# Performance work log

Measured on AMD Instinct MI355X. Metric: run time of the kernel, lower is better.

Reference implementation:

```python
import jax, jax.numpy as jnp
import numpy as np

N = 50000
E = 800000
IN_CH = 128
HIDDEN = 32
HEADS = 4
OUT_CH = 64
NEG_SLOPE = 0.2


def setup_inputs() -> dict:
    key = jax.random.key(0)
    ks = jax.random.split(key, 12)
    x = jax.random.normal(ks[0], (N, IN_CH), dtype=jnp.float32)
    edge_index = jax.random.randint(ks[1], (2, E), 0, N, dtype=jnp.int64)
    # layer 1: GATConv(IN_CH, HIDDEN, heads=4, concat=True)
    s1 = 1.0 / np.sqrt(IN_CH)
    W1 = jax.random.normal(ks[2], (IN_CH, HEADS * HIDDEN), dtype=jnp.float32) * s1
    att_src1 = jax.random.normal(ks[3], (HEADS, HIDDEN), dtype=jnp.float32) * 0.1
    att_dst1 = jax.random.normal(ks[4], (HEADS, HIDDEN), dtype=jnp.float32) * 0.1
    b1 = jnp.zeros((HEADS * HIDDEN,), dtype=jnp.float32)
    # layer 2: GATConv(HEADS*HIDDEN, OUT_CH, heads=1, concat=False)
    s2 = 1.0 / np.sqrt(HEADS * HIDDEN)
    W2 = jax.random.normal(ks[5], (HEADS * HIDDEN, OUT_CH), dtype=jnp.float32) * s2
    att_src2 = jax.random.normal(ks[6], (1, OUT_CH), dtype=jnp.float32) * 0.1
    att_dst2 = jax.random.normal(ks[7], (1, OUT_CH), dtype=jnp.float32) * 0.1
    b2 = jnp.zeros((OUT_CH,), dtype=jnp.float32)
    return {"x": x, "edge_index": edge_index, "W1": W1, "att_src1": att_src1,
            "att_dst1": att_dst1, "b1": b1, "W2": W2, "att_src2": att_src2,
            "att_dst2": att_dst2, "b2": b2}


def gat_conv(x, src, dst, W, a_src, a_dst, bias, heads, out_ch, concat):
    n = x.shape[0]
    h = (x @ W).reshape(n, heads, out_ch)               # [N, H, C]
    alpha_s = jnp.sum(h * a_src[None], axis=-1)          # [N, H]
    alpha_d = jnp.sum(h * a_dst[None], axis=-1)          # [N, H]
    e = alpha_s[src] + alpha_d[dst]                      # [E, H]
    e = jnp.where(e > 0, e, NEG_SLOPE * e)               # leaky_relu(0.2)
    # segment softmax over incoming edges of each dst node
    e_max = jax.ops.segment_max(e, dst, num_segments=n)
    e_max = jnp.where(jnp.isfinite(e_max), e_max, 0.0)
    ex = jnp.exp(e - e_max[dst])
    denom = jax.ops.segment_sum(ex, dst, num_segments=n)
    alpha = ex / (denom[dst] + 1e-16)                    # [E, H]
    msg = h[src] * alpha[:, :, None]                     # [E, H, C]
    out = jax.ops.segment_sum(msg, dst, num_segments=n)  # [N, H, C]
    if concat:
        out = out.reshape(n, heads * out_ch)
    else:
        out = out.mean(axis=1)
    return out + bias


def reference(x, edge_index, W1, att_src1, att_dst1, b1, W2, att_src2, att_dst2, b2):
    n = x.shape[0]
    loop = jnp.arange(n, dtype=edge_index.dtype)
    src = jnp.concatenate([edge_index[0], loop])  # add self-loops (PyG default)
    dst = jnp.concatenate([edge_index[1], loop])
    h = gat_conv(x, src, dst, W1, att_src1, att_dst1, b1, HEADS, HIDDEN, True)
    h = jax.nn.elu(h)
    return gat_conv(h, src, dst, W2, att_src2, att_dst2, b2, 1, OUT_CH, False)
```

## Files before the change

### kernel.cpp

```cpp
#include <hip/hip_runtime.h>

#define NN    50000
#define NE    800000
#define NET   850000
#define NBUCK ((NN + 255) / 256)
#define MAXB  8192

typedef __fp16 half2_t __attribute__((ext_vector_type(2)));
typedef _Float16 half8 __attribute__((ext_vector_type(8)));
typedef float floatx4 __attribute__((ext_vector_type(4)));

__device__ __forceinline__ float lrelu(float v) { return fmaxf(v, 0.2f * v); }
__device__ __forceinline__ unsigned pk16(float a, float b) {
    half2_t h = __builtin_amdgcn_cvt_pkrtz(a, b);
    return __builtin_bit_cast(unsigned, h);
}
__device__ __forceinline__ float2 unpk16(unsigned u) {
    half2_t h = __builtin_bit_cast(half2_t, u);
    return make_float2((float)h.x, (float)h.y);
}

__global__ __launch_bounds__(256) void gemm1_mfma_kernel(
    const float* __restrict__ x, const _Float16* __restrict__ w1t,
    const float* __restrict__ att_s, const float* __restrict__ att_d,
    _Float16* __restrict__ h1h, float* __restrict__ as, float* __restrict__ ad)
{
    __shared__ _Float16 hs[64 * 128];
    const int t    = threadIdx.x;
    const int lane = t & 63;
    const int m    = lane & 15;
    const int q    = lane >> 4;
    const int wv   = t >> 6;
    const int gr0  = blockIdx.x * 64;
    const int rbase = gr0 + wv * 16;

    const int rme = rbase + m;
    const int rc  = rme < NN ? rme : NN - 1;
    const float* ap = x + (size_t)rc * 128 + q * 8;

    floatx4 acc[8];
#pragma unroll
    for (int nt = 0; nt < 8; nt++) acc[nt] = (floatx4){0.f, 0.f, 0.f, 0.f};

#pragma unroll
    for (int ks = 0; ks < 4; ks++) {
        const float4 f0 = *(const float4*)(ap + ks * 32);
        const float4 f1 = *(const float4*)(ap + ks * 32 + 4);
        const uint4 au = make_uint4(pk16(f0.x, f0.y), pk16(f0.z, f0.w),
                                    pk16(f1.x, f1.y), pk16(f1.z, f1.w));
        const half8 a = __builtin_bit_cast(half8, au);
#pragma unroll
        for (int nt = 0; nt < 8; nt++) {
            const half8 b = *(const half8*)(w1t + (nt * 16 + m) * 128 + ks * 32 + q * 8);
            acc[nt] = __builtin_amdgcn_mfma_f32_16x16x32_f16(a, b, acc[nt], 0, 0, 0);
        }
    }

    const int lrow0 = wv * 16 + q * 4;
#pragma unroll
    for (int nt = 0; nt < 8; nt++)
#pragma unroll
        for (int r = 0; r < 4; r++)
            hs[(lrow0 + r) * 128 + nt * 16 + m] = (_Float16)acc[nt][r];
    __syncthreads();

#pragma unroll
    for (int i = t; i < 1024; i += 256) {
        const int row = i >> 4;
        if (gr0 + row < NN)
            ((half8*)h1h)[(size_t)(gr0 + row) * 16 + (i & 15)] = ((const half8*)hs)[i];
    }

    const int arow = t >> 2, hd = t & 3;
    const int grow = gr0 + arow;
    float ps = 0.f, pd = 0.f;
    const half8*  hp8 = (const half8*)(hs + arow * 128 + hd * 32);
    const float4* s4  = (const float4*)(att_s + hd * 32);
    const float4* d4  = (const float4*)(att_d + hd * 32);
#pragma unroll
    for (int cc = 0; cc < 4; cc++) {
        const half8 hv = hp8[cc];
        const float4 a = s4[cc * 2], b = s4[cc * 2 + 1];
        const float4 c = d4[cc * 2], e = d4[cc * 2 + 1];
        ps += (float)hv[0]*a.x + (float)hv[1]*a.y + (float)hv[2]*a.z + (float)hv[3]*a.w
            + (float)hv[4]*b.x + (float)hv[5]*b.y + (float)hv[6]*b.z + (float)hv[7]*b.w;
        pd += (float)hv[0]*c.x + (float)hv[1]*c.y + (float)hv[2]*c.z + (float)hv[3]*c.w
            + (float)hv[4]*e.x + (float)hv[5]*e.y + (float)hv[6]*e.z + (float)hv[7]*e.w;
    }
    if (grow < NN) {
        as[grow * 4 + hd] = ps;
        ad[grow * 4 + hd] = pd;
    }
}

__global__ __launch_bounds__(256) void gemm2_mfma_kernel(
    const _Float16* __restrict__ ah, const _Float16* __restrict__ w2t,
    const float* __restrict__ att_s, const float* __restrict__ att_d,
    _Float16* __restrict__ h2h, float* __restrict__ as, float* __restrict__ ad)
{
    __shared__ _Float16 hs[64 * 64];
    const int t    = threadIdx.x;
    const int lane = t & 63;
    const int m    = lane & 15;
    const int q    = lane >> 4;
    const int wv   = t >> 6;
    const int gr0  = blockIdx.x * 64;
    const int rbase = gr0 + wv * 16;

    const int rme = rbase + m;
    const int rc  = rme < NN ? rme : NN - 1;
    const _Float16* ap = ah + (size_t)rc * 128 + q * 8;

    floatx4 acc[4];
#pragma unroll
    for (int nt = 0; nt < 4; nt++) acc[nt] = (floatx4){0.f, 0.f, 0.f, 0.f};

#pragma unroll
    for (int ks = 0; ks < 4; ks++) {
        const half8 a = *(const half8*)(ap + ks * 32);
#pragma unroll
        for (int nt = 0; nt < 4; nt++) {
            const half8 b = *(const half8*)(w2t + (nt * 16 + m) * 128 + ks * 32 + q * 8);
            acc[nt] = __builtin_amdgcn_mfma_f32_16x16x32_f16(a, b, acc[nt], 0, 0, 0);
        }
    }

    const int lrow0 = wv * 16 + q * 4;
#pragma unroll
    for (int nt = 0; nt < 4; nt++)
#pragma unroll
        for (int r = 0; r < 4; r++)
            hs[(lrow0 + r) * 64 + nt * 16 + m] = (_Float16)acc[nt][r];
    __syncthreads();

#pragma unroll
    for (int i = t; i < 512; i += 256) {
        const int row = i >> 3;
        if (gr0 + row < NN)
            ((half8*)h2h)[(size_t)(gr0 + row) * 8 + (i & 7)] = ((const half8*)hs)[i];
    }

    const int arow = t >> 2, sg = t & 3;
    const int grow = gr0 + arow;
    float ps = 0.f, pd = 0.f;
    const half8*  hp8 = (const half8*)(hs + arow * 64 + sg * 16);
    const float4* s4  = (const float4*)(att_s + sg * 16);
    const float4* d4  = (const float4*)(att_d + sg * 16);
#pragma unroll
    for (int cc = 0; cc < 2; cc++) {
        const half8 hv = hp8[cc];
        const float4 a = s4[cc * 2], b = s4[cc * 2 + 1];
        const float4 c = d4[cc * 2], e = d4[cc * 2 + 1];
        ps += (float)hv[0]*a.x + (float)hv[1]*a.y + (float)hv[2]*a.z + (float)hv[3]*a.w
            + (float)hv[4]*b.x + (float)hv[5]*b.y + (float)hv[6]*b.z + (float)hv[7]*b.w;
        pd += (float)hv[0]*c.x + (float)hv[1]*c.y + (float)hv[2]*c.z + (float)hv[3]*c.w
            + (float)hv[4]*e.x + (float)hv[5]*e.y + (float)hv[6]*e.z + (float)hv[7]*e.w;
    }
    ps += __shfl_down(ps, 2);  pd += __shfl_down(pd, 2);
    ps += __shfl_down(ps, 1);  pd += __shfl_down(pd, 1);
    if (sg == 0 && grow < NN) { as[grow] = ps; ad[grow] = pd; }
}

__global__ __launch_bounds__(1024) void bin_kernel(const int* __restrict__ ei,
                                                   const float* __restrict__ W1,
                                                   const float* __restrict__ W2,
                                                   _Float16* __restrict__ w1t,
                                                   _Float16* __restrict__ w2t,
                                                   int* __restrict__ bcnt,
                                                   unsigned* __restrict__ pairs)
{
    if (blockIdx.x < 24) {
        const int idx = blockIdx.x * 1024 + threadIdx.x;
        if (idx < 16384) {
            const int k = idx >> 7, n = idx & 127;
            w1t[n * 128 + k] = (_Float16)W1[idx];
        } else {
            const int j = idx - 16384;
            const int k = j >> 6, n = j & 63;
            w2t[n * 128 + k] = (_Float16)W2[j];
        }
    }

    __shared__ int hist[NBUCK], base[NBUCK], cur[NBUCK];
    const int t = threadIdx.x;
    if (t < NBUCK) { hist[t] = 0; cur[t] = 0; }
    __syncthreads();
    const int e = blockIdx.x * 1024 + t;
    int s = 0, d = 0, bk = 0;
    const bool ok = e < NET;
    if (ok) {
        if (e < NE) { s = ei[e]; d = ei[NE + e]; } else { s = d = e - NE; }
        bk = d >> 8;
        atomicAdd(&hist[bk], 1);
    }
    __syncthreads();
    if (t < NBUCK && hist[t]) base[t] = atomicAdd(&bcnt[t], hist[t]);
    __syncthreads();
    if (ok) {
        const int r = atomicAdd(&cur[bk], 1);
        pairs[(size_t)bk * MAXB + base[bk] + r] =
            (unsigned)s | ((unsigned)(d & 255) << 16);
    }
}

__global__ __launch_bounds__(1024) void bsort_kernel(
    const int* __restrict__ bcnt, const unsigned* __restrict__ pairs,
    int* __restrict__ row_beg, int* __restrict__ row_end,
    int* __restrict__ col)
{
    __shared__ int hist[256], cur[256], sh[256];
    __shared__ int outl[MAXB];
    const int b = blockIdx.x, t = threadIdx.x;
    const int m = bcnt[b];
    const int gbase = b * MAXB;
    if (t < 256) hist[t] = 0;
    __syncthreads();
    for (int i = t; i < m; i += 1024)
        atomicAdd(&hist[pairs[gbase + i] >> 16], 1);
    __syncthreads();
    if (t < 256) sh[t] = hist[t];
    __syncthreads();
#pragma unroll
    for (int off = 1; off < 256; off <<= 1) {
        int u = (t < 256 && t >= off) ? sh[t - off] : 0;
        __syncthreads();
        if (t < 256) sh[t] += u;
        __syncthreads();
    }
    if (t < 256) {
        const int ex = sh[t] - hist[t];
        cur[t] = ex;
        const int node = (b << 8) + t;
        if (node < NN) {
            row_beg[node] = gbase + ex;
            row_end[node] = gbase + ex + hist[t];
        }
    }
    __syncthreads();
    for (int i = t; i < m; i += 1024) {
        const unsigned p = pairs[gbase + i];
        const int r = atomicAdd(&cur[p >> 16], 1);
        outl[r] = (int)(p & 0xFFFFu);
    }
    __syncthreads();
    for (int i = t; i < m; i += 1024) col[gbase + i] = outl[i];
}

__global__ __launch_bounds__(256) void agg1_fused_kernel(
    const int* __restrict__ row_beg, const int* __restrict__ row_end,
    const int* __restrict__ col, const unsigned* __restrict__ hh,
    const float* __restrict__ as1, const float* __restrict__ ad1,
    const float* __restrict__ b1, unsigned* __restrict__ acth)
{
    __shared__ float wbuf[4][64 * 4];
    const int wv   = threadIdx.x >> 6;
    const int d    = __builtin_amdgcn_readfirstlane((blockIdx.x * 256 + threadIdx.x) >> 6);
    const int lane = threadIdx.x & 63;
    const int head = lane >> 4;
    const int beg = row_beg[d], end = row_end[d];
    const float4 ad4 = ((const float4*)ad1)[d];
    float* wb = wbuf[wv];

    float acc0 = 0.f, acc1 = 0.f, den = 0.f;

    for (int jb = beg; jb < end; jb += 64) {
        const int cnt = min(64, end - jb);
        {
            const int sl = col[jb + min(lane, cnt - 1)];
            const float4 a = ((const float4*)as1)[sl];
            float4 w4;
            w4.x = __expf(lrelu(a.x + ad4.x));
            w4.y = __expf(lrelu(a.y + ad4.y));
            w4.z = __expf(lrelu(a.z + ad4.z));
            w4.w = __expf(lrelu(a.w + ad4.w));
            ((float4*)wb)[lane] = w4;
        }
        __asm__ volatile("s_waitcnt lgkmcnt(0)" ::: "memory");

        int k = 0;
        for (; k + 16 <= cnt; k += 16) {
            float    w[16];
            unsigned g[16];
#pragma unroll
            for (int u = 0; u < 16; u++) {
                const int s = col[jb + k + u];
                w[u] = wb[(k + u) * 4 + head];
                g[u] = hh[s * 64 + lane];
            }
#pragma unroll
            for (int u = 0; u < 16; u++) {
                const float2 g2 = unpk16(g[u]);
                den  += w[u];
                acc0 += w[u] * g2.x;
                acc1 += w[u] * g2.y;
            }
        }
        for (; k + 4 <= cnt; k += 4) {
            float    w[4];
            unsigned g[4];
#pragma unroll
            for (int u = 0; u < 4; u++) {
                const int s = col[jb + k + u];
                w[u] = wb[(k + u) * 4 + head];
                g[u] = hh[s * 64 + lane];
            }
#pragma unroll
            for (int u = 0; u < 4; u++) {
                const float2 g2 = unpk16(g[u]);
                den  += w[u];
                acc0 += w[u] * g2.x;
                acc1 += w[u] * g2.y;
            }
        }
        for (; k < cnt; k++) {
            const float w = wb[k * 4 + head];
            const float2 g2 = unpk16(hh[col[jb + k] * 64 + lane]);
            den  += w;
            acc0 += w * g2.x;
            acc1 += w * g2.y;
        }
        __asm__ volatile("" ::: "memory");
    }
    const float2 bb  = ((const float2*)b1)[lane];
    const float  inv = 1.f / (den + 1e-16f);
    float v0 = acc0 * inv + bb.x;
    float v1 = acc1 * inv + bb.y;
    v0 = v0 > 0.f ? v0 : (__expf(v0) - 1.f);
    v1 = v1 > 0.f ? v1 : (__expf(v1) - 1.f);
    acth[d * 64 + lane] = pk16(v0, v1);
}

__global__ __launch_bounds__(256) void agg2_fused_kernel(
    const int* __restrict__ row_beg, const int* __restrict__ row_end,
    const int* __restrict__ col, const _Float16* __restrict__ h,
    const float* __restrict__ as2, const float* __restrict__ ad2,
    const float* __restrict__ b2, float* __restrict__ out)
{
    __shared__ float wbuf[4][64];
    const int wv   = threadIdx.x >> 6;
    const int d    = __builtin_amdgcn_readfirstlane((blockIdx.x * 256 + threadIdx.x) >> 6);
    const int lane = threadIdx.x & 63;
    const int beg = row_beg[d], end = row_end[d];
    const float add = ad2[d];
    float* wb = wbuf[wv];

    float acc = 0.f, den = 0.f;

    for (int jb = beg; jb < end; jb += 64) {
        const int cnt = min(64, end - jb);
        {
            const int sl = col[jb + min(lane, cnt - 1)];
            wb[lane] = __expf(lrelu(as2[sl] + add));
        }
        __asm__ volatile("s_waitcnt lgkmcnt(0)" ::: "memory");

        int k = 0;
        for (; k + 16 <= cnt; k += 16) {
            float w[16], g[16];
#pragma unroll
            for (int u = 0; u < 16; u++) {
                const int s = col[jb + k + u];
                w[u] = wb[k + u];
                g[u] = (float)h[s * 64 + lane];
            }
#pragma unroll
            for (int u = 0; u < 16; u++) {
                den += w[u];
                acc += w[u] * g[u];
            }
        }
        for (; k + 4 <= cnt; k += 4) {
            float w[4], g[4];
#pragma unroll
            for (int u = 0; u < 4; u++) {
                const int s = col[jb + k + u];
                w[u] = wb[k + u];
                g[u] = (float)h[s * 64 + lane];
            }
#pragma unroll
            for (int u = 0; u < 4; u++) {
                den += w[u];
                acc += w[u] * g[u];
            }
        }
        for (; k < cnt; k++) {
            const float w = wb[k];
            den += w;
            acc += w * (float)h[col[jb + k] * 64 + lane];
        }
        __asm__ volatile("" ::: "memory");
    }
    out[d * 64 + lane] = acc / (den + 1e-16f) + b2[lane];
}

extern "C" void kernel_launch(void* const* d_in, const int* in_sizes, int n_in,
                              void* d_out, int out_size, void* d_ws, size_t ws_size,
                              hipStream_t stream)
{
    const float* x    = (const float*)d_in[0];
    const int*   ei   = (const int*)  d_in[1];
    const float* W1   = (const float*)d_in[2];
    const float* at_s1= (const float*)d_in[3];
    const float* at_d1= (const float*)d_in[4];
    const float* b1   = (const float*)d_in[5];
    const float* W2   = (const float*)d_in[6];
    const float* at_s2= (const float*)d_in[7];
    const float* at_d2= (const float*)d_in[8];
    const float* b2   = (const float*)d_in[9];
    float*       out  = (float*)d_out;

    const size_t NPAD = (size_t)NBUCK * MAXB;

    float* fw   = (float*)d_ws;
    float* as1  = fw;
    float* ad1  = as1  + NN * 4;
    float* as2  = ad1  + NN * 4;
    float* ad2  = as2  + NN;
    _Float16* h1h   = (_Float16*)(ad2 + NN);
    _Float16* act1h = h1h  + (size_t)NN * 128;
    _Float16* h2h   = act1h+ (size_t)NN * 128;
    _Float16* w1t   = h2h  + (size_t)NN * 64;
    _Float16* w2t   = w1t  + 16384;
    int*   row_beg = (int*)(w2t + 8192);
    int*   row_end = row_beg + NN;
    int*   col     = row_end + NN;
    int*   bcnt    = col + NPAD;
    unsigned* pairs = (unsigned*)(bcnt + 256);

    hipMemsetAsync(bcnt, 0, 256 * sizeof(int), stream);

    const int eg1024 = (NET + 1023) / 1024;
    const int gemm_grid = (NN + 63) / 64;
    const int node_wave_grid = NN / 4;

    bin_kernel  <<<eg1024, 1024, 0, stream>>>(ei, W1, W2, w1t, w2t, bcnt, pairs);
    bsort_kernel<<<NBUCK, 1024, 0, stream>>>(bcnt, pairs, row_beg, row_end, col);

    gemm1_mfma_kernel<<<gemm_grid, 256, 0, stream>>>(x, w1t, at_s1, at_d1, h1h, as1, ad1);
    agg1_fused_kernel<<<node_wave_grid, 256, 0, stream>>>(row_beg, row_end, col,
                        (const unsigned*)h1h, as1, ad1, b1, (unsigned*)act1h);

    gemm2_mfma_kernel<<<gemm_grid, 256, 0, stream>>>(act1h, w2t, at_s2, at_d2, h2h, as2, ad2);
    agg2_fused_kernel<<<node_wave_grid, 256, 0, stream>>>(row_beg, row_end, col,
                        h2h, as2, ad2, b2, out);
}
```

Before: 211.5 us.

## Split each wavefront across four edges with wide vector gathers in aggregation

Both aggregation kernels now split each 64-lane wavefront into four 16-lane groups. Each group processes a different incoming edge and gathers that source row with one 16-byte load (layer 1) or one 8-byte load (layer 2) per lane, instead of every lane loading a single 4-byte or 2-byte element for every edge. Per-lane accumulators are then combined across the groups with xor shuffles before normalisation, bias and ELU. The aim is fewer, wider gather instructions and more edges in flight per wavefront. In exchange it needs more accumulator registers, adds a cross-lane reduction, and pads the tail edges with zero weight.

Measured after the change: 213.0 us. Within noise of the previous version (+0.7%).

```diff
diff --git a/kernel.cpp b/kernel.cpp
--- a/kernel.cpp
+++ b/kernel.cpp
@@ -256,12 +256,16 @@
     const int wv   = threadIdx.x >> 6;
     const int d    = __builtin_amdgcn_readfirstlane((blockIdx.x * 256 + threadIdx.x) >> 6);
     const int lane = threadIdx.x & 63;
-    const int head = lane >> 4;
+    const int c    = lane & 15;
+    const int p    = lane >> 4;
+    const int head = c >> 2;
     const int beg = row_beg[d], end = row_end[d];
     const float4 ad4 = ((const float4*)ad1)[d];
     float* wb = wbuf[wv];
 
-    float acc0 = 0.f, acc1 = 0.f, den = 0.f;
+    float acc0 = 0.f, acc1 = 0.f, acc2 = 0.f, acc3 = 0.f;
+    float acc4 = 0.f, acc5 = 0.f, acc6 = 0.f, acc7 = 0.f;
+    float den = 0.f;
 
     for (int jb = beg; jb < end; jb += 64) {
         const int cnt = min(64, end - jb);
@@ -279,55 +283,82 @@
 
         int k = 0;
         for (; k + 16 <= cnt; k += 16) {
-            float    w[16];
-            unsigned g[16];
-#pragma unroll
-            for (int u = 0; u < 16; u++) {
-                const int s = col[jb + k + u];
-                w[u] = wb[(k + u) * 4 + head];
-                g[u] = hh[s * 64 + lane];
+            float w[4];
+            uint4 g[4];
+#pragma unroll
+            for (int u = 0; u < 4; u++) {
+                const int e0 = jb + k + 4 * u;
+                const int sA = col[e0], sB = col[e0 + 1];
+                const int sC = col[e0 + 2], sD = col[e0 + 3];
+                int s  = (p & 1) ? sB : sA;
+                const int s2 = (p & 1) ? sD : sC;
+                s = (p & 2) ? s2 : s;
+                w[u] = wb[(k + 4 * u + p) * 4 + head];
+                g[u] = *(const uint4*)(hh + (size_t)s * 64 + 4 * c);
             }
 #pragma unroll
-            for (int u = 0; u < 16; u++) {
-                const float2 g2 = unpk16(g[u]);
+            for (int u = 0; u < 4; u++) {
+                const float2 g0 = unpk16(g[u].x), g1 = unpk16(g[u].y);
+                const float2 g2 = unpk16(g[u].z), g3 = unpk16(g[u].w);
                 den  += w[u];
-                acc0 += w[u] * g2.x;
-                acc1 += w[u] * g2.y;
+                acc0 += w[u] * g0.x;  acc1 += w[u] * g0.y;
+                acc2 += w[u] * g1.x;  acc3 += w[u] * g1.y;
+                acc4 += w[u] * g2.x;  acc5 += w[u] * g2.y;
+                acc6 += w[u] * g3.x;  acc7 += w[u] * g3.y;
             }
         }
-        for (; k + 4 <= cnt; k += 4) {
-            float    w[4];
-            unsigned g[4];
-#pragma unroll
-            for (int u = 0; u < 4; u++) {
-                const int s = col[jb + k + u];
-                w[u] = wb[(k + u) * 4 + head];
-                g[u] = hh[s * 64 + lane];
-            }
-#pragma unroll
-            for (int u = 0; u < 4; u++) {
-                const float2 g2 = unpk16(g[u]);
-                den  += w[u];
-                acc0 += w[u] * g2.x;
-                acc1 += w[u] * g2.y;
-            }
-        }
-        for (; k < cnt; k++) {
-            const float w = wb[k * 4 + head];
-            const float2 g2 = unpk16(hh[col[jb + k] * 64 + lane]);
+        for (; k < cnt; k += 4) {
+            const int sA = col[jb + k];
+            const int sB = col[jb + min(k + 1, cnt - 1)];
+            const int sC = col[jb + min(k + 2, cnt - 1)];
+            const int sD = col[jb + min(k + 3, cnt - 1)];
+            int s  = (p & 1) ? sB : sA;
+            const int s2 = (p & 1) ? sD : sC;
+            s = (p & 2) ? s2 : s;
+            const float w = (k + p < cnt) ? wb[(k + p) * 4 + head] : 0.f;
+            const uint4 gv = *(const uint4*)(hh + (size_t)s * 64 + 4 * c);
+            const float2 g0 = unpk16(gv.x), g1 = unpk16(gv.y);
+            const float2 g2 = unpk16(gv.z), g3 = unpk16(gv.w);
             den  += w;
-            acc0 += w * g2.x;
-            acc1 += w * g2.y;
+            acc0 += w * g0.x;  acc1 += w * g0.y;
+            acc2 += w * g1.x;  acc3 += w * g1.y;
+            acc4 += w * g2.x;  acc5 += w * g2.y;
+            acc6 += w * g3.x;  acc7 += w * g3.y;
         }
         __asm__ volatile("" ::: "memory");
     }
-    const float2 bb  = ((const float2*)b1)[lane];
+    acc0 += __shfl_xor(acc0, 16);  acc0 += __shfl_xor(acc0, 32);
+    acc1 += __shfl_xor(acc1, 16);  acc1 += __shfl_xor(acc1, 32);
+    acc2 += __shfl_xor(acc2, 16);  acc2 += __shfl_xor(acc2, 32);
+    acc3 += __shfl_xor(acc3, 16);  acc3 += __shfl_xor(acc3, 32);
+    acc4 += __shfl_xor(acc4, 16);  acc4 += __shfl_xor(acc4, 32);
+    acc5 += __shfl_xor(acc5, 16);  acc5 += __shfl_xor(acc5, 32);
+    acc6 += __shfl_xor(acc6, 16);  acc6 += __shfl_xor(acc6, 32);
+    acc7 += __shfl_xor(acc7, 16);  acc7 += __shfl_xor(acc7, 32);
+    den  += __shfl_xor(den, 16);   den  += __shfl_xor(den, 32);
+
+    const float4 bbA = ((const float4*)b1)[2 * c];
+    const float4 bbB = ((const float4*)b1)[2 * c + 1];
     const float  inv = 1.f / (den + 1e-16f);
-    float v0 = acc0 * inv + bb.x;
-    float v1 = acc1 * inv + bb.y;
+    float v0 = acc0 * inv + bbA.x;
+    float v1 = acc1 * inv + bbA.y;
+    float v2 = acc2 * inv + bbA.z;
+    float v3 = acc3 * inv + bbA.w;
+    float v4 = acc4 * inv + bbB.x;
+    float v5 = acc5 * inv + bbB.y;
+    float v6 = acc6 * inv + bbB.z;
+    float v7 = acc7 * inv + bbB.w;
     v0 = v0 > 0.f ? v0 : (__expf(v0) - 1.f);
     v1 = v1 > 0.f ? v1 : (__expf(v1) - 1.f);
-    acth[d * 64 + lane] = pk16(v0, v1);
+    v2 = v2 > 0.f ? v2 : (__expf(v2) - 1.f);
+    v3 = v3 > 0.f ? v3 : (__expf(v3) - 1.f);
+    v4 = v4 > 0.f ? v4 : (__expf(v4) - 1.f);
+    v5 = v5 > 0.f ? v5 : (__expf(v5) - 1.f);
+    v6 = v6 > 0.f ? v6 : (__expf(v6) - 1.f);
+    v7 = v7 > 0.f ? v7 : (__expf(v7) - 1.f);
+    const float o0 = (p == 0) ? v0 : (p == 1) ? v2 : (p == 2) ? v4 : v6;
+    const float o1 = (p == 0) ? v1 : (p == 1) ? v3 : (p == 2) ? v5 : v7;
+    acth[d * 64 + 4 * c + p] = pk16(o0, o1);
 }
 
 __global__ __launch_bounds__(256) void agg2_fused_kernel(
@@ -340,11 +371,14 @@
     const int wv   = threadIdx.x >> 6;
     const int d    = __builtin_amdgcn_readfirstlane((blockIdx.x * 256 + threadIdx.x) >> 6);
     const int lane = threadIdx.x & 63;
+    const int c    = lane & 15;
+    const int p    = lane >> 4;
     const int beg = row_beg[d], end = row_end[d];
     const float add = ad2[d];
     float* wb = wbuf[wv];
-
-    float acc = 0.f, den = 0.f;
+    const unsigned* __restrict__ h2 = (const unsigned*)h;
+
+    float acc0 = 0.f, acc1 = 0.f, acc2 = 0.f, acc3 = 0.f, den = 0.f;
 
     for (int jb = beg; jb < end; jb += 64) {
         const int cnt = min(64, end - jb);
@@ -356,41 +390,53 @@
 
         int k = 0;
         for (; k + 16 <= cnt; k += 16) {
-            float w[16], g[16];
-#pragma unroll
-            for (int u = 0; u < 16; u++) {
-                const int s = col[jb + k + u];
-                w[u] = wb[k + u];
-                g[u] = (float)h[s * 64 + lane];
+            float w[4];
+            uint2 g[4];
+#pragma unroll
+            for (int u = 0; u < 4; u++) {
+                const int e0 = jb + k + 4 * u;
+                const int sA = col[e0], sB = col[e0 + 1];
+                const int sC = col[e0 + 2], sD = col[e0 + 3];
+                int s  = (p & 1) ? sB : sA;
+                const int s2 = (p & 1) ? sD : sC;
+                s = (p & 2) ? s2 : s;
+                w[u] = wb[k + 4 * u + p];
+                g[u] = *(const uint2*)(h2 + (size_t)s * 32 + 2 * c);
             }
 #pragma unroll
-            for (int u = 0; u < 16; u++) {
-                den += w[u];
-                acc += w[u] * g[u];
+            for (int u = 0; u < 4; u++) {
+                const float2 g0 = unpk16(g[u].x), g1 = unpk16(g[u].y);
+                den  += w[u];
+                acc0 += w[u] * g0.x;  acc1 += w[u] * g0.y;
+                acc2 += w[u] * g1.x;  acc3 += w[u] * g1.y;
             }
         }
-        for (; k + 4 <= cnt; k += 4) {
-            float w[4], g[4];
-#pragma unroll
-            for (int u = 0; u < 4; u++) {
-                const int s = col[jb + k + u];
-                w[u] = wb[k + u];
-                g[u] = (float)h[s * 64 + lane];
-            }
-#pragma unroll
-            for (int u = 0; u < 4; u++) {
-                den += w[u];
-                acc += w[u] * g[u];
-            }
-        }
-        for (; k < cnt; k++) {
-            const float w = wb[k];
-            den += w;
-            acc += w * (float)h[col[jb + k] * 64 + lane];
+        for (; k < cnt; k += 4) {
+            const int sA = col[jb + k];
+            const int sB = col[jb + min(k + 1, cnt - 1)];
+            const int sC = col[jb + min(k + 2, cnt - 1)];
+            const int sD = col[jb + min(k + 3, cnt - 1)];
+            int s  = (p & 1) ? sB : sA;
+            const int s2 = (p & 1) ? sD : sC;
+            s = (p & 2) ? s2 : s;
+            const float w = (k + p < cnt) ? wb[k + p] : 0.f;
+            const uint2 gv = *(const uint2*)(h2 + (size_t)s * 32 + 2 * c);
+            const float2 g0 = unpk16(gv.x), g1 = unpk16(gv.y);
+            den  += w;
+            acc0 += w * g0.x;  acc1 += w * g0.y;
+            acc2 += w * g1.x;  acc3 += w * g1.y;
         }
         __asm__ volatile("" ::: "memory");
     }
-    out[d * 64 + lane] = acc / (den + 1e-16f) + b2[lane];
+    acc0 += __shfl_xor(acc0, 16);  acc0 += __shfl_xor(acc0, 32);
+    acc1 += __shfl_xor(acc1, 16);  acc1 += __shfl_xor(acc1, 32);
+    acc2 += __shfl_xor(acc2, 16);  acc2 += __shfl_xor(acc2, 32);
+    acc3 += __shfl_xor(acc3, 16);  acc3 += __shfl_xor(acc3, 32);
+    den  += __shfl_xor(den, 16);   den  += __shfl_xor(den, 32);
+
+    const float inv = 1.f / (den + 1e-16f);
+    const float a = (p == 0) ? acc0 : (p == 1) ? acc1 : (p == 2) ? acc2 : acc3;
+    out[d * 64 + 4 * c + p] = a * inv + b2[4 * c + p];
 }
 
 extern "C" void kernel_launch(void* const* d_in, const int* in_sizes, int n_in,
```

## Stage GEMM weights in swizzled LDS and use persistent binning with padded counters

Applied to the files above, without the earlier changes.

Both GEMM kernels now copy the transposed fp16 weight matrix into LDS with an XOR swizzle and prefetch the A rows into registers before the barrier. This replaces repeated global/L2 reads of B fragments with bank-conflict-free shared-memory reads. The bin kernel becomes a grid-stride loop over 256 blocks, so fewer global atomics hit the bucket counters. The counters are also padded to 16 ints apart to avoid contention on shared cache lines. The cost is extra LDS per GEMM block, which may lower occupancy, and the edge indices are read twice in binning.

Result: faster. 186.1 us (median of 2 runs) (-12.0%).

```diff
diff --git a/kernel.cpp b/kernel.cpp
--- a/kernel.cpp
+++ b/kernel.cpp
@@ -5,6 +5,7 @@
 #define NET   850000
 #define NBUCK ((NN + 255) / 256)
 #define MAXB  8192
+#define BINB  256
 
 typedef __fp16 half2_t __attribute__((ext_vector_type(2)));
 typedef _Float16 half8 __attribute__((ext_vector_type(8)));
@@ -25,6 +26,7 @@
     const float* __restrict__ att_s, const float* __restrict__ att_d,
     _Float16* __restrict__ h1h, float* __restrict__ as, float* __restrict__ ad)
 {
+    __shared__ _Float16 lw[128 * 128];
     __shared__ _Float16 hs[64 * 128];
     const int t    = threadIdx.x;
     const int lane = t & 63;
@@ -38,20 +40,40 @@
     const int rc  = rme < NN ? rme : NN - 1;
     const float* ap = x + (size_t)rc * 128 + q * 8;
 
+    float4 f0[4], f1[4];
+#pragma unroll
+    for (int ks = 0; ks < 4; ks++) {
+        f0[ks] = *(const float4*)(ap + ks * 32);
+        f1[ks] = *(const float4*)(ap + ks * 32 + 4);
+    }
+
+    {
+        const int kb = t & 15;
+        const int n0 = t >> 4;
+#pragma unroll
+        for (int it = 0; it < 8; it++) {
+            const int n = n0 + it * 16;
+            const uint4 v = *(const uint4*)(w1t + n * 128 + kb * 8);
+            *(uint4*)((char*)lw + n * 256 + ((kb * 16) ^ ((n & 7) << 4))) = v;
+        }
+    }
+    __syncthreads();
+
     floatx4 acc[8];
 #pragma unroll
     for (int nt = 0; nt < 8; nt++) acc[nt] = (floatx4){0.f, 0.f, 0.f, 0.f};
 
+    const int swz = (m & 7) << 4;
 #pragma unroll
     for (int ks = 0; ks < 4; ks++) {
-        const float4 f0 = *(const float4*)(ap + ks * 32);
-        const float4 f1 = *(const float4*)(ap + ks * 32 + 4);
-        const uint4 au = make_uint4(pk16(f0.x, f0.y), pk16(f0.z, f0.w),
-                                    pk16(f1.x, f1.y), pk16(f1.z, f1.w));
+        const uint4 au = make_uint4(pk16(f0[ks].x, f0[ks].y), pk16(f0[ks].z, f0[ks].w),
+                                    pk16(f1[ks].x, f1[ks].y), pk16(f1[ks].z, f1[ks].w));
         const half8 a = __builtin_bit_cast(half8, au);
 #pragma unroll
         for (int nt = 0; nt < 8; nt++) {
-            const half8 b = *(const half8*)(w1t + (nt * 16 + m) * 128 + ks * 32 + q * 8);
+            const int n = nt * 16 + m;
+            const half8 b = *(const half8*)((const char*)lw + n * 256 +
+                                            ((ks * 64 + q * 16) ^ swz));
             acc[nt] = __builtin_amdgcn_mfma_f32_16x16x32_f16(a, b, acc[nt], 0, 0, 0);
         }
     }
@@ -98,6 +120,7 @@
     const float* __restrict__ att_s, const float* __restrict__ att_d,
     _Float16* __restrict__ h2h, float* __restrict__ as, float* __restrict__ ad)
 {
+    __shared__ _Float16 lw[64 * 128];
     __shared__ _Float16 hs[64 * 64];
     const int t    = threadIdx.x;
     const int lane = t & 63;
@@ -111,17 +134,35 @@
     const int rc  = rme < NN ? rme : NN - 1;
     const _Float16* ap = ah + (size_t)rc * 128 + q * 8;
 
+    half8 av[4];
+#pragma unroll
+    for (int ks = 0; ks < 4; ks++) av[ks] = *(const half8*)(ap + ks * 32);
+
+    {
+        const int kb = t & 15;
+        const int n0 = t >> 4;
+#pragma unroll
+        for (int it = 0; it < 4; it++) {
+            const int n = n0 + it * 16;
+            const uint4 v = *(const uint4*)(w2t + n * 128 + kb * 8);
+            *(uint4*)((char*)lw + n * 256 + ((kb * 16) ^ ((n & 7) << 4))) = v;
+        }
+    }
+    __syncthreads();
+
     floatx4 acc[4];
 #pragma unroll
     for (int nt = 0; nt < 4; nt++) acc[nt] = (floatx4){0.f, 0.f, 0.f, 0.f};
 
+    const int swz = (m & 7) << 4;
 #pragma unroll
     for (int ks = 0; ks < 4; ks++) {
-        const half8 a = *(const half8*)(ap + ks * 32);
 #pragma unroll
         for (int nt = 0; nt < 4; nt++) {
-            const half8 b = *(const half8*)(w2t + (nt * 16 + m) * 128 + ks * 32 + q * 8);
-            acc[nt] = __builtin_amdgcn_mfma_f32_16x16x32_f16(a, b, acc[nt], 0, 0, 0);
+            const int n = nt * 16 + m;
+            const half8 b = *(const half8*)((const char*)lw + n * 256 +
+                                            ((ks * 64 + q * 16) ^ swz));
+            acc[nt] = __builtin_amdgcn_mfma_f32_16x16x32_f16(av[ks], b, acc[nt], 0, 0, 0);
         }
     }
 
@@ -185,18 +226,18 @@
     const int t = threadIdx.x;
     if (t < NBUCK) { hist[t] = 0; cur[t] = 0; }
     __syncthreads();
-    const int e = blockIdx.x * 1024 + t;
-    int s = 0, d = 0, bk = 0;
-    const bool ok = e < NET;
-    if (ok) {
+
+    for (int e = blockIdx.x * 1024 + t; e < NET; e += BINB * 1024) {
+        const int d = (e < NE) ? ei[NE + e] : (e - NE);
+        atomicAdd(&hist[d >> 8], 1);
+    }
+    __syncthreads();
+    if (t < NBUCK && hist[t]) base[t] = atomicAdd(&bcnt[t * 16], hist[t]);
+    __syncthreads();
+    for (int e = blockIdx.x * 1024 + t; e < NET; e += BINB * 1024) {
+        int s, d;
         if (e < NE) { s = ei[e]; d = ei[NE + e]; } else { s = d = e - NE; }
-        bk = d >> 8;
-        atomicAdd(&hist[bk], 1);
-    }
-    __syncthreads();
-    if (t < NBUCK && hist[t]) base[t] = atomicAdd(&bcnt[t], hist[t]);
-    __syncthreads();
-    if (ok) {
+        const int bk = d >> 8;
         const int r = atomicAdd(&cur[bk], 1);
         pairs[(size_t)bk * MAXB + base[bk] + r] =
             (unsigned)s | ((unsigned)(d & 255) << 16);
@@ -211,7 +252,7 @@
     __shared__ int hist[256], cur[256], sh[256];
     __shared__ int outl[MAXB];
     const int b = blockIdx.x, t = threadIdx.x;
-    const int m = bcnt[b];
+    const int m = bcnt[b * 16];
     const int gbase = b * MAXB;
     if (t < 256) hist[t] = 0;
     __syncthreads();
@@ -425,15 +466,14 @@
     int*   row_end = row_beg + NN;
     int*   col     = row_end + NN;
     int*   bcnt    = col + NPAD;
-    unsigned* pairs = (unsigned*)(bcnt + 256);
-
-    hipMemsetAsync(bcnt, 0, 256 * sizeof(int), stream);
-
-    const int eg1024 = (NET + 1023) / 1024;
+    unsigned* pairs = (unsigned*)(bcnt + 4096);
+
+    hipMemsetAsync(bcnt, 0, 4096 * sizeof(int), stream);
+
     const int gemm_grid = (NN + 63) / 64;
     const int node_wave_grid = NN / 4;
 
-    bin_kernel  <<<eg1024, 1024, 0, stream>>>(ei, W1, W2, w1t, w2t, bcnt, pairs);
+    bin_kernel  <<<BINB, 1024, 0, stream>>>(ei, W1, W2, w1t, w2t, bcnt, pairs);
     bsort_kernel<<<NBUCK, 1024, 0, stream>>>(bcnt, pairs, row_beg, row_end, col);
 
     gemm1_mfma_kernel<<<gemm_grid, 256, 0, stream>>>(x, w1t, at_s1, at_d1, h1h, as1, ad1);
```
